# Kernel tuning notes

Hardware: AMD Instinct MI355X
Metric: run time of the kernel (lower is better)

The kernel has to match this reference:

```python
import jax, jax.numpy as jnp
import numpy as np

N_NODES = 100000


def _graph_conv(x, W, b, src, dst, norm):
    # DGL GraphConv(norm='left'): scale source features by 1/out_degree,
    # aggregate (sum over incoming edges). in_feats > out_feats so weight
    # multiply happens before aggregation (mathematically equivalent either way).
    h = x @ W  # [N, out]
    msg = (h * norm[:, None])[src]  # gather per-edge messages [E, out]
    agg = jax.ops.segment_sum(msg, dst, num_segments=N_NODES)
    return agg + b


def setup_inputs() -> dict:
    key = jax.random.key(0)
    ks = jax.random.split(key, 10)
    in_f, hid_f, out_f = 256, 128, 64
    n_edges = 1_600_000
    feat = jax.random.normal(ks[0], (N_NODES, in_f), dtype=jnp.float32)
    src = jax.random.randint(ks[1], (n_edges,), 0, N_NODES, dtype=jnp.int32)
    dst = jax.random.randint(ks[2], (n_edges,), 0, N_NODES, dtype=jnp.int32)
    noise = jax.random.normal(ks[3], (N_NODES, out_f), dtype=jnp.float32)
    s1 = 1.0 / np.sqrt(in_f)
    s2 = 1.0 / np.sqrt(hid_f)
    W_shared = jax.random.uniform(ks[4], (in_f, hid_f), minval=-s1, maxval=s1, dtype=jnp.float32)
    b_shared = jnp.zeros((hid_f,), jnp.float32)
    W_mu = jax.random.uniform(ks[5], (hid_f, out_f), minval=-s2, maxval=s2, dtype=jnp.float32)
    b_mu = jnp.zeros((out_f,), jnp.float32)
    W_ls = jax.random.uniform(ks[6], (hid_f, out_f), minval=-s2, maxval=s2, dtype=jnp.float32)
    b_ls = jnp.zeros((out_f,), jnp.float32)
    return {"feat": feat, "W_shared": W_shared, "b_shared": b_shared,
            "W_mu": W_mu, "b_mu": b_mu, "W_ls": W_ls, "b_ls": b_ls,
            "noise": noise, "src": src, "dst": dst}


def reference(feat, W_shared, b_shared, W_mu, b_mu, W_ls, b_ls, noise, src, dst):
    # left-norm: 1 / out_degree (clamped to >= 1, as DGL does)
    deg_out = jax.ops.segment_sum(jnp.ones_like(src, jnp.float32), src,
                                  num_segments=N_NODES)
    norm = 1.0 / jnp.maximum(deg_out, 1.0)
    # shared first GraphConv with ReLU activation
    h = jax.nn.relu(_graph_conv(feat, W_shared, b_shared, src, dst, norm))
    # two heads (no activation)
    mu = _graph_conv(h, W_mu, b_mu, src, dst, norm)
    log_sigma = _graph_conv(h, W_ls, b_ls, src, dst, norm)
    # reparameterized sample
    return mu + noise * jnp.exp(log_sigma)
```

## Files before the change

kernel.cpp:

```cpp
#include <hip/hip_runtime.h>
#include <hip/hip_bf16.h>
#include <math.h>

typedef __attribute__((ext_vector_type(8))) short short8;
typedef __attribute__((ext_vector_type(4))) float f32x4;

__device__ __forceinline__ unsigned short f2bf(float f) {
    unsigned int u = __float_as_uint(f);
    u += 0x7FFF + ((u >> 16) & 1);
    return (unsigned short)(u >> 16);
}
__device__ __forceinline__ float b2f(unsigned short s) {
    return __uint_as_float(((unsigned int)s) << 16);
}
__device__ __forceinline__ unsigned int f2bf2(float a, float b) {
    __hip_bfloat162 h = __float22bfloat162_rn(make_float2(a, b));
    return *(unsigned int*)&h;
}
__device__ __forceinline__ void gl_lds16(const void* g, void* l) {
    __builtin_amdgcn_global_load_lds(
        (const __attribute__((address_space(1))) void*)g,
        (__attribute__((address_space(3))) void*)l, 16, 0, 0);
}

#define EB 8192
#define BSH 10
#define NBKT 128

__global__ __launch_bounds__(256)
void k1_hist(const int* __restrict__ src, const int* __restrict__ dst,
             int* __restrict__ bhist, int E) {
    __shared__ int hist[256];
    int t = threadIdx.x;
    hist[t] = 0;
    __syncthreads();
    int base = blockIdx.x * EB;
    int end = min(base + EB, E);
    for (int e = base + 4 * t; e < end; e += 1024) {
        if (e + 3 < end) {
            int4 d4 = *(const int4*)&dst[e];
            int4 s4 = *(const int4*)&src[e];
            atomicAdd(&hist[d4.x >> BSH], 1);
            atomicAdd(&hist[d4.y >> BSH], 1);
            atomicAdd(&hist[d4.z >> BSH], 1);
            atomicAdd(&hist[d4.w >> BSH], 1);
            atomicAdd(&hist[128 + (s4.x >> BSH)], 1);
            atomicAdd(&hist[128 + (s4.y >> BSH)], 1);
            atomicAdd(&hist[128 + (s4.z >> BSH)], 1);
            atomicAdd(&hist[128 + (s4.w >> BSH)], 1);
        } else {
            for (int q = e; q < end; ++q) {
                atomicAdd(&hist[dst[q] >> BSH], 1);
                atomicAdd(&hist[128 + (src[q] >> BSH)], 1);
            }
        }
    }
    __syncthreads();
    bhist[(size_t)blockIdx.x * 256 + t] = hist[t];
}

__global__ __launch_bounds__(256)
void kc1_totals(const int* __restrict__ bhist, int* __restrict__ totals, int PB) {
    int t = threadIdx.x;
    int slice = (PB + 7) / 8;
    int b0 = blockIdx.x * slice;
    int b1 = min(b0 + slice, PB);
    int s = 0;
    for (int blk = b0; blk < b1; ++blk) s += bhist[(size_t)blk * 256 + t];
    if (s) atomicAdd(&totals[t], s);
}

__global__ __launch_bounds__(256)
void kc2_scan2(const int* __restrict__ totals, int* __restrict__ bbase_d,
               int* __restrict__ bbase_s) {
    __shared__ int s[256];
    int t = threadIdx.x;
    int v = totals[t];
    s[t] = v;
    __syncthreads();
    for (int off = 1; off < 128; off <<= 1) {
        int u = ((t & 127) >= off) ? s[t - off] : 0;
        __syncthreads();
        s[t] += u;
        __syncthreads();
    }
    int excl = s[t] - v;
    if (t < 128) bbase_d[t] = excl;
    else bbase_s[t - 128] = excl;
}

__global__ __launch_bounds__(256)
void kc3_boff(const int* __restrict__ bhist, const int* __restrict__ bbase_d,
              const int* __restrict__ bbase_s, int* __restrict__ boffT, int PB) {
    __shared__ int sums[256];
    int b = blockIdx.x;
    int t = threadIdx.x;
    int v = (t < PB) ? bhist[(size_t)t * 256 + b] : 0;
    sums[t] = v;
    __syncthreads();
    for (int off = 1; off < 256; off <<= 1) {
        int u = (t >= off) ? sums[t - off] : 0;
        __syncthreads();
        sums[t] += u;
        __syncthreads();
    }
    int base = (b < 128) ? bbase_d[b] : bbase_s[b - 128];
    if (t < PB) boffT[(size_t)b * PB + t] = base + sums[t] - v;
}

__global__ __launch_bounds__(256)
void k2_scatter(const int* __restrict__ src, const int* __restrict__ dst,
                const int* __restrict__ boffT, int2* __restrict__ parr,
                int* __restrict__ sarr, int E, int PB) {
    __shared__ int cnt[256];
    int t = threadIdx.x;
    int blk = blockIdx.x;
    cnt[t] = boffT[(size_t)t * PB + blk];
    __syncthreads();
    int base = blk * EB;
    int end = min(base + EB, E);
    for (int e = base + 4 * t; e < end; e += 1024) {
        if (e + 3 < end) {
            int4 s4 = *(const int4*)&src[e];
            int4 d4 = *(const int4*)&dst[e];
            int p0 = atomicAdd(&cnt[d4.x >> BSH], 1); parr[p0] = make_int2(s4.x, d4.x);
            int p1 = atomicAdd(&cnt[d4.y >> BSH], 1); parr[p1] = make_int2(s4.y, d4.y);
            int p2 = atomicAdd(&cnt[d4.z >> BSH], 1); parr[p2] = make_int2(s4.z, d4.z);
            int p3 = atomicAdd(&cnt[d4.w >> BSH], 1); parr[p3] = make_int2(s4.w, d4.w);
            int q0 = atomicAdd(&cnt[128 + (s4.x >> BSH)], 1); sarr[q0] = s4.x;
            int q1 = atomicAdd(&cnt[128 + (s4.y >> BSH)], 1); sarr[q1] = s4.y;
            int q2 = atomicAdd(&cnt[128 + (s4.z >> BSH)], 1); sarr[q2] = s4.z;
            int q3 = atomicAdd(&cnt[128 + (s4.w >> BSH)], 1); sarr[q3] = s4.w;
        } else {
            for (int q = e; q < end; ++q) {
                int sv = src[q], dv = dst[q];
                int pd = atomicAdd(&cnt[dv >> BSH], 1);
                parr[pd] = make_int2(sv, dv);
                int ps = atomicAdd(&cnt[128 + (sv >> BSH)], 1);
                sarr[ps] = sv;
            }
        }
    }
}

__global__ __launch_bounds__(1024)
void k3_dst(const int2* __restrict__ parr, const int* __restrict__ totals,
            const int* __restrict__ bbase_d, int* __restrict__ row_off,
            int* __restrict__ col, int N, int E) {
    __shared__ int hist[1024], sc[1024];
    int b = blockIdx.x, t = threadIdx.x;
    if (b == 0 && t == 0) row_off[N] = E;
    int ne = totals[b];
    int ebase = bbase_d[b];
    hist[t] = 0;
    __syncthreads();
    for (int i = t; i < ne; i += 1024)
        atomicAdd(&hist[parr[ebase + i].y & 1023], 1);
    __syncthreads();
    int h = hist[t];
    sc[t] = h;
    __syncthreads();
    for (int off = 1; off < 1024; off <<= 1) {
        int u = (t >= off) ? sc[t - off] : 0;
        __syncthreads();
        sc[t] += u;
        __syncthreads();
    }
    int excl = sc[t] - h;
    int node = b * 1024 + t;
    if (node < N) row_off[node] = ebase + excl;
    hist[t] = ebase + excl;
    __syncthreads();
    for (int i = t; i < ne; i += 1024) {
        int2 pr = parr[ebase + i];
        int slot = atomicAdd(&hist[pr.y & 1023], 1);
        col[slot] = pr.x;
    }
}

__global__ __launch_bounds__(1024)
void k3_src(const int* __restrict__ sarr, const int* __restrict__ totals_s,
            const int* __restrict__ bbase_s, float* __restrict__ norm, int N) {
    __shared__ int hist[1024];
    int b = blockIdx.x, t = threadIdx.x;
    int ne = totals_s[b];
    int sb = bbase_s[b];
    hist[t] = 0;
    __syncthreads();
    for (int i = t; i < ne; i += 1024)
        atomicAdd(&hist[sarr[sb + i] & 1023], 1);
    __syncthreads();
    int node = b * 1024 + t;
    if (node < N) {
        int d = hist[t];
        norm[node] = 1.0f / (float)(d > 1 ? d : 1);
    }
}

__global__ __launch_bounds__(256)
void k_wprep(const float* __restrict__ Wsh, const float* __restrict__ Wmu,
             const float* __restrict__ Wls, unsigned short* __restrict__ W1T,
             unsigned short* __restrict__ W2T) {
    int b = blockIdx.x, t = threadIdx.x;
    if (b < 128) {
        W1T[(size_t)b * 256 + t] = f2bf(Wsh[(size_t)t * 128 + b]);
    } else {
        int n = b - 128;
        if (t < 128) {
            float v = (n < 64) ? Wmu[(size_t)t * 64 + n]
                               : Wls[(size_t)t * 64 + (n - 64)];
            W2T[(size_t)n * 128 + t] = f2bf(v);
        }
    }
}

__global__ __launch_bounds__(256)
void k_gemm1(const float* __restrict__ A, int M,
             const unsigned short* __restrict__ W1T,
             const float* __restrict__ norm, unsigned short* __restrict__ outb) {
    __shared__ char ldsA[64 * 1040];
    const int w = threadIdx.x >> 6;
    const int lane = threadIdx.x & 63;
    const int quad = lane >> 4;
    const int l16 = lane & 15;
    const int cl = w * 16 + l16;
    const int r0 = blockIdx.x * 64;

#pragma unroll
    for (int i = 0; i < 16; ++i) {
        int row = r0 + w * 16 + i;
        if (row >= M) row = M - 1;
        const char* g = (const char*)A + (size_t)row * 1024 + lane * 16;
        char* l = ldsA + (w * 16 + i) * 1040 + lane * 16;
        gl_lds16(g, l);
    }

    short8 bw[2][8];
#pragma unroll
    for (int hf = 0; hf < 2; ++hf) {
        const unsigned short* wp = W1T + (size_t)(hf * 64 + cl) * 256 + quad * 8;
#pragma unroll
        for (int ks = 0; ks < 8; ++ks)
            bw[hf][ks] = *(const short8*)(wp + ks * 32);
    }
    __syncthreads();

    f32x4 acc[4][2];
#pragma unroll
    for (int m = 0; m < 4; ++m) {
        acc[m][0] = (f32x4){0.f, 0.f, 0.f, 0.f};
        acc[m][1] = (f32x4){0.f, 0.f, 0.f, 0.f};
    }
#pragma unroll
    for (int ks = 0; ks < 8; ++ks) {
#pragma unroll
        for (int m = 0; m < 4; ++m) {
            const float* pr = (const float*)(ldsA + (m * 16 + l16) * 1040 +
                                             (ks * 32 + quad * 8) * 4);
            float4 x = *(const float4*)pr;
            float4 y = *(const float4*)(pr + 4);
            union { short8 v; unsigned int u[4]; } c;
            c.u[0] = f2bf2(x.x, x.y);
            c.u[1] = f2bf2(x.z, x.w);
            c.u[2] = f2bf2(y.x, y.y);
            c.u[3] = f2bf2(y.z, y.w);
            acc[m][0] = __builtin_amdgcn_mfma_f32_16x16x32_bf16(bw[0][ks], c.v, acc[m][0], 0, 0, 0);
            acc[m][1] = __builtin_amdgcn_mfma_f32_16x16x32_bf16(bw[1][ks], c.v, acc[m][1], 0, 0, 0);
        }
    }
    const int colbase = w * 16 + quad * 4;
#pragma unroll
    for (int m = 0; m < 4; ++m) {
        int row = r0 + m * 16 + l16;
        if (row < M) {
            float nm = norm[row];
            ushort4 o0, o1;
            o0.x = f2bf(acc[m][0][0] * nm); o0.y = f2bf(acc[m][0][1] * nm);
            o0.z = f2bf(acc[m][0][2] * nm); o0.w = f2bf(acc[m][0][3] * nm);
            o1.x = f2bf(acc[m][1][0] * nm); o1.y = f2bf(acc[m][1][1] * nm);
            o1.z = f2bf(acc[m][1][2] * nm); o1.w = f2bf(acc[m][1][3] * nm);
            *(ushort4*)&outb[(size_t)row * 128 + colbase] = o0;
            *(ushort4*)&outb[(size_t)row * 128 + 64 + colbase] = o1;
        }
    }
}

__global__ __launch_bounds__(256)
void k_gemm2(const unsigned short* __restrict__ A, int M,
             const unsigned short* __restrict__ W2T,
             const float* __restrict__ norm, unsigned short* __restrict__ outb) {
    __shared__ char ldsB[16 * 1040];
    const int w = threadIdx.x >> 6;
    const int lane = threadIdx.x & 63;
    const int quad = lane >> 4;
    const int l16 = lane & 15;
    const int cl = w * 16 + l16;
    const int r0 = blockIdx.x * 64;

#pragma unroll
    for (int i = 0; i < 4; ++i) {
        int c = w * 4 + i;
        int crow = r0 + c * 4;
        if (crow + 4 > M) crow = M - 4;
        const char* g = (const char*)A + (size_t)crow * 256 + lane * 16;
        char* l = ldsB + c * 1040 + lane * 16;
        gl_lds16(g, l);
    }

    short8 bw[2][4];
#pragma unroll
    for (int hf = 0; hf < 2; ++hf) {
        const unsigned short* wp = W2T + (size_t)(hf * 64 + cl) * 128 + quad * 8;
#pragma unroll
        for (int ks = 0; ks < 4; ++ks)
            bw[hf][ks] = *(const short8*)(wp + ks * 32);
    }
    __syncthreads();

    f32x4 acc[4][2];
#pragma unroll
    for (int m = 0; m < 4; ++m) {
        acc[m][0] = (f32x4){0.f, 0.f, 0.f, 0.f};
        acc[m][1] = (f32x4){0.f, 0.f, 0.f, 0.f};
    }
#pragma unroll
    for (int ks = 0; ks < 4; ++ks) {
#pragma unroll
        for (int m = 0; m < 4; ++m) {
            int row = m * 16 + l16;
            short8 af = *(const short8*)(ldsB + (row >> 2) * 1040 + (row & 3) * 256 +
                                         (ks * 32 + quad * 8) * 2);
            acc[m][0] = __builtin_amdgcn_mfma_f32_16x16x32_bf16(bw[0][ks], af, acc[m][0], 0, 0, 0);
            acc[m][1] = __builtin_amdgcn_mfma_f32_16x16x32_bf16(bw[1][ks], af, acc[m][1], 0, 0, 0);
        }
    }
    const int colbase = w * 16 + quad * 4;
#pragma unroll
    for (int m = 0; m < 4; ++m) {
        int row = r0 + m * 16 + l16;
        if (row < M) {
            float nm = norm[row];
            ushort4 o0, o1;
            o0.x = f2bf(acc[m][0][0] * nm); o0.y = f2bf(acc[m][0][1] * nm);
            o0.z = f2bf(acc[m][0][2] * nm); o0.w = f2bf(acc[m][0][3] * nm);
            o1.x = f2bf(acc[m][1][0] * nm); o1.y = f2bf(acc[m][1][1] * nm);
            o1.z = f2bf(acc[m][1][2] * nm); o1.w = f2bf(acc[m][1][3] * nm);
            *(ushort4*)&outb[(size_t)row * 128 + colbase] = o0;
            *(ushort4*)&outb[(size_t)row * 128 + 64 + colbase] = o1;
        }
    }
}

__global__ __launch_bounds__(256)
void k_spmm_relu(const int* __restrict__ row_off, const int* __restrict__ col,
                 const unsigned short* __restrict__ hxb, const float* __restrict__ bias,
                 unsigned short* __restrict__ hb, int N) {
    int g = (blockIdx.x * blockDim.x + threadIdx.x) >> 5;
    int l = threadIdx.x & 31;
    if (g >= N) return;
    int e0 = row_off[g], e1 = row_off[g + 1];
    const ushort4* base = (const ushort4*)hxb;
    float4 acc = make_float4(0.f, 0.f, 0.f, 0.f);
    int e = e0;
    for (; e + 7 < e1; e += 8) {
        ushort4 v0 = base[(size_t)col[e] * 32 + l];
        ushort4 v1 = base[(size_t)col[e + 1] * 32 + l];
        ushort4 v2 = base[(size_t)col[e + 2] * 32 + l];
        ushort4 v3 = base[(size_t)col[e + 3] * 32 + l];
        ushort4 v4 = base[(size_t)col[e + 4] * 32 + l];
        ushort4 v5 = base[(size_t)col[e + 5] * 32 + l];
        ushort4 v6 = base[(size_t)col[e + 6] * 32 + l];
        ushort4 v7 = base[(size_t)col[e + 7] * 32 + l];
        acc.x += ((b2f(v0.x) + b2f(v1.x)) + (b2f(v2.x) + b2f(v3.x))) +
                 ((b2f(v4.x) + b2f(v5.x)) + (b2f(v6.x) + b2f(v7.x)));
        acc.y += ((b2f(v0.y) + b2f(v1.y)) + (b2f(v2.y) + b2f(v3.y))) +
                 ((b2f(v4.y) + b2f(v5.y)) + (b2f(v6.y) + b2f(v7.y)));
        acc.z += ((b2f(v0.z) + b2f(v1.z)) + (b2f(v2.z) + b2f(v3.z))) +
                 ((b2f(v4.z) + b2f(v5.z)) + (b2f(v6.z) + b2f(v7.z)));
        acc.w += ((b2f(v0.w) + b2f(v1.w)) + (b2f(v2.w) + b2f(v3.w))) +
                 ((b2f(v4.w) + b2f(v5.w)) + (b2f(v6.w) + b2f(v7.w)));
    }
    for (; e + 1 < e1; e += 2) {
        ushort4 a = base[(size_t)col[e] * 32 + l];
        ushort4 b = base[(size_t)col[e + 1] * 32 + l];
        acc.x += b2f(a.x) + b2f(b.x);
        acc.y += b2f(a.y) + b2f(b.y);
        acc.z += b2f(a.z) + b2f(b.z);
        acc.w += b2f(a.w) + b2f(b.w);
    }
    if (e < e1) {
        ushort4 a = base[(size_t)col[e] * 32 + l];
        acc.x += b2f(a.x); acc.y += b2f(a.y); acc.z += b2f(a.z); acc.w += b2f(a.w);
    }
    float4 bi = ((const float4*)bias)[l];
    ushort4 r;
    r.x = f2bf(fmaxf(acc.x + bi.x, 0.f));
    r.y = f2bf(fmaxf(acc.y + bi.y, 0.f));
    r.z = f2bf(fmaxf(acc.z + bi.z, 0.f));
    r.w = f2bf(fmaxf(acc.w + bi.w, 0.f));
    ((ushort4*)hb)[(size_t)g * 32 + l] = r;
}

__global__ __launch_bounds__(256)
void k_spmm_out(const int* __restrict__ row_off, const int* __restrict__ col,
                const unsigned short* __restrict__ hcb, const float* __restrict__ bmu,
                const float* __restrict__ bls, const float* __restrict__ noise,
                float* __restrict__ out, int N) {
    int g = (blockIdx.x * blockDim.x + threadIdx.x) >> 5;
    int l = threadIdx.x & 31;
    if (g >= N) return;
    int e0 = row_off[g], e1 = row_off[g + 1];
    const ushort4* base = (const ushort4*)hcb;
    float4 acc = make_float4(0.f, 0.f, 0.f, 0.f);
    int e = e0;
    for (; e + 7 < e1; e += 8) {
        ushort4 v0 = base[(size_t)col[e] * 32 + l];
        ushort4 v1 = base[(size_t)col[e + 1] * 32 + l];
        ushort4 v2 = base[(size_t)col[e + 2] * 32 + l];
        ushort4 v3 = base[(size_t)col[e + 3] * 32 + l];
        ushort4 v4 = base[(size_t)col[e + 4] * 32 + l];
        ushort4 v5 = base[(size_t)col[e + 5] * 32 + l];
        ushort4 v6 = base[(size_t)col[e + 6] * 32 + l];
        ushort4 v7 = base[(size_t)col[e + 7] * 32 + l];
        acc.x += ((b2f(v0.x) + b2f(v1.x)) + (b2f(v2.x) + b2f(v3.x))) +
                 ((b2f(v4.x) + b2f(v5.x)) + (b2f(v6.x) + b2f(v7.x)));
        acc.y += ((b2f(v0.y) + b2f(v1.y)) + (b2f(v2.y) + b2f(v3.y))) +
                 ((b2f(v4.y) + b2f(v5.y)) + (b2f(v6.y) + b2f(v7.y)));
        acc.z += ((b2f(v0.z) + b2f(v1.z)) + (b2f(v2.z) + b2f(v3.z))) +
                 ((b2f(v4.z) + b2f(v5.z)) + (b2f(v6.z) + b2f(v7.z)));
        acc.w += ((b2f(v0.w) + b2f(v1.w)) + (b2f(v2.w) + b2f(v3.w))) +
                 ((b2f(v4.w) + b2f(v5.w)) + (b2f(v6.w) + b2f(v7.w)));
    }
    for (; e + 1 < e1; e += 2) {
        ushort4 a = base[(size_t)col[e] * 32 + l];
        ushort4 b = base[(size_t)col[e + 1] * 32 + l];
        acc.x += b2f(a.x) + b2f(b.x);
        acc.y += b2f(a.y) + b2f(b.y);
        acc.z += b2f(a.z) + b2f(b.z);
        acc.w += b2f(a.w) + b2f(b.w);
    }
    if (e < e1) {
        ushort4 a = base[(size_t)col[e] * 32 + l];
        acc.x += b2f(a.x); acc.y += b2f(a.y); acc.z += b2f(a.z); acc.w += b2f(a.w);
    }
    int lane64 = threadIdx.x & 63;
    int p = (lane64 + 16) & 63;
    float lx = __shfl(acc.x, p, 64);
    float ly = __shfl(acc.y, p, 64);
    float lz = __shfl(acc.z, p, 64);
    float lw = __shfl(acc.w, p, 64);
    if (l < 16) {
        float4 bm = ((const float4*)bmu)[l];
        float4 bl = ((const float4*)bls)[l];
        float4 nz = ((const float4*)noise)[(size_t)g * 16 + l];
        float4 o;
        o.x = (acc.x + bm.x) + nz.x * expf(lx + bl.x);
        o.y = (acc.y + bm.y) + nz.y * expf(ly + bl.y);
        o.z = (acc.z + bm.z) + nz.z * expf(lz + bl.z);
        o.w = (acc.w + bm.w) + nz.w * expf(lw + bl.w);
        ((float4*)out)[(size_t)g * 16 + l] = o;
    }
}

static inline char* align64(char* p) {
    return (char*)(((uintptr_t)p + 63) & ~(uintptr_t)63);
}

extern "C" void kernel_launch(void* const* d_in, const int* in_sizes, int n_in,
                              void* d_out, int out_size, void* d_ws, size_t ws_size,
                              hipStream_t stream) {
    const float* feat  = (const float*)d_in[0];
    const float* Wsh   = (const float*)d_in[1];
    const float* bsh   = (const float*)d_in[2];
    const float* Wmu   = (const float*)d_in[3];
    const float* bmu   = (const float*)d_in[4];
    const float* Wls   = (const float*)d_in[5];
    const float* bls   = (const float*)d_in[6];
    const float* noise = (const float*)d_in[7];
    const int*   src   = (const int*)d_in[8];
    const int*   dst   = (const int*)d_in[9];
    float* out = (float*)d_out;

    const int N = in_sizes[0] / 256;
    const int E = in_sizes[8];
    const int PB = (E + EB - 1) / EB;

    char* p = (char*)d_ws;
    float* norm   = (float*)p;                  p += (size_t)N * 4;         p = align64(p);
    int* row_off  = (int*)p;                    p += (size_t)(N + 4) * 4;   p = align64(p);
    int* totals   = (int*)p;                    p += 256 * 4;
    int* bbase_d  = (int*)p;                    p += 128 * 4;
    int* bbase_s  = (int*)p;                    p += 128 * 4;               p = align64(p);
    unsigned short* W1T = (unsigned short*)p;   p += (size_t)128 * 256 * 2;
    unsigned short* W2T = (unsigned short*)p;   p += (size_t)128 * 128 * 2;
    p = align64(p);
    int* bhist    = (int*)p;                    p += (size_t)PB * 256 * 4;  p = align64(p);
    int* boffT    = (int*)p;                    p += (size_t)256 * PB * 4;  p = align64(p);
    int2* parr    = (int2*)p;                   p += (size_t)E * 8;
    int* sarr     = (int*)p;                    p += (size_t)E * 4;
    int* col      = (int*)p;                    p += (size_t)E * 4;         p = align64(p);
    unsigned short* hxb = (unsigned short*)p;
    unsigned short* hb  = (unsigned short*)d_out;

    hipMemsetAsync(totals, 0, 256 * sizeof(int), stream);
    k_wprep<<<256, 256, 0, stream>>>(Wsh, Wmu, Wls, W1T, W2T);
    k1_hist<<<PB, 256, 0, stream>>>(src, dst, bhist, E);
    kc1_totals<<<8, 256, 0, stream>>>(bhist, totals, PB);
    kc2_scan2<<<1, 256, 0, stream>>>(totals, bbase_d, bbase_s);
    kc3_boff<<<256, 256, 0, stream>>>(bhist, bbase_d, bbase_s, boffT, PB);
    k2_scatter<<<PB, 256, 0, stream>>>(src, dst, boffT, parr, sarr, E, PB);
    k3_dst<<<NBKT, 1024, 0, stream>>>(parr, totals, bbase_d, row_off, col, N, E);
    k3_src<<<NBKT, 1024, 0, stream>>>(sarr, totals + 128, bbase_s, norm, N);

    int gtiles = (N + 63) / 64;
    k_gemm1<<<gtiles, 256, 0, stream>>>(feat, N, W1T, norm, hxb);
    k_spmm_relu<<<(N * 32 + 255) / 256, 256, 0, stream>>>(row_off, col, hxb, bsh, hb, N);
    k_gemm2<<<gtiles, 256, 0, stream>>>(hb, N, W2T, norm, hxb);
    k_spmm_out<<<(N * 32 + 255) / 256, 256, 0, stream>>>(row_off, col, hxb, bmu, bls, noise, out, N);
}
```

Baseline: 450.0 us.

## Use 256 finer CSR buckets, pack edge pairs into 32 bits, merge scan kernels

Bucket width for the CSR build drops from 1024 to 512 nodes, giving 256 dst/src buckets so the per-bucket kernels launch more, smaller blocks. Edge pairs are packed into one int (17-bit src plus 9-bit local dst) and the src-degree array stores only 16-bit local ids, cutting scatter write traffic and later read traffic. The totals reduction and bucket scan are merged into one single-block kernel, removing a memset and a launch. The packing assumes node ids fit in 17 bits and the merged kernel runs on only one block, which may serialize the reduction over bhist.

```diff
diff --git a/kernel.cpp b/kernel.cpp
--- a/kernel.cpp
+++ b/kernel.cpp
@@ -24,15 +24,15 @@
 }
 
 #define EB 8192
-#define BSH 10
-#define NBKT 128
+#define BSH 9
+#define NBKT 256
 
 __global__ __launch_bounds__(256)
 void k1_hist(const int* __restrict__ src, const int* __restrict__ dst,
              int* __restrict__ bhist, int E) {
-    __shared__ int hist[256];
+    __shared__ int hist[512];
     int t = threadIdx.x;
-    hist[t] = 0;
+    hist[t] = 0; hist[t + 256] = 0;
     __syncthreads();
     int base = blockIdx.x * EB;
     int end = min(base + EB, E);
@@ -44,49 +44,54 @@
             atomicAdd(&hist[d4.y >> BSH], 1);
             atomicAdd(&hist[d4.z >> BSH], 1);
             atomicAdd(&hist[d4.w >> BSH], 1);
-            atomicAdd(&hist[128 + (s4.x >> BSH)], 1);
-            atomicAdd(&hist[128 + (s4.y >> BSH)], 1);
-            atomicAdd(&hist[128 + (s4.z >> BSH)], 1);
-            atomicAdd(&hist[128 + (s4.w >> BSH)], 1);
+            atomicAdd(&hist[256 + (s4.x >> BSH)], 1);
+            atomicAdd(&hist[256 + (s4.y >> BSH)], 1);
+            atomicAdd(&hist[256 + (s4.z >> BSH)], 1);
+            atomicAdd(&hist[256 + (s4.w >> BSH)], 1);
         } else {
             for (int q = e; q < end; ++q) {
                 atomicAdd(&hist[dst[q] >> BSH], 1);
-                atomicAdd(&hist[128 + (src[q] >> BSH)], 1);
+                atomicAdd(&hist[256 + (src[q] >> BSH)], 1);
             }
         }
     }
     __syncthreads();
-    bhist[(size_t)blockIdx.x * 256 + t] = hist[t];
-}
-
-__global__ __launch_bounds__(256)
-void kc1_totals(const int* __restrict__ bhist, int* __restrict__ totals, int PB) {
+    int* o = bhist + (size_t)blockIdx.x * 512;
+    o[t] = hist[t];
+    o[t + 256] = hist[t + 256];
+}
+
+__global__ __launch_bounds__(1024)
+void kc12(const int* __restrict__ bhist, int* __restrict__ totals,
+          int* __restrict__ bbase_d, int* __restrict__ bbase_s, int PB) {
+    __shared__ int part[1024];
+    __shared__ int s[512];
     int t = threadIdx.x;
-    int slice = (PB + 7) / 8;
-    int b0 = blockIdx.x * slice;
-    int b1 = min(b0 + slice, PB);
-    int s = 0;
-    for (int blk = b0; blk < b1; ++blk) s += bhist[(size_t)blk * 256 + t];
-    if (s) atomicAdd(&totals[t], s);
-}
-
-__global__ __launch_bounds__(256)
-void kc2_scan2(const int* __restrict__ totals, int* __restrict__ bbase_d,
-               int* __restrict__ bbase_s) {
-    __shared__ int s[256];
-    int t = threadIdx.x;
-    int v = totals[t];
-    s[t] = v;
-    __syncthreads();
-    for (int off = 1; off < 128; off <<= 1) {
-        int u = ((t & 127) >= off) ? s[t - off] : 0;
+    int bin = t & 511, half = t >> 9;
+    int sum = 0;
+    for (int blk = half; blk < PB; blk += 2)
+        sum += bhist[(size_t)blk * 512 + bin];
+    part[t] = sum;
+    __syncthreads();
+    int v = 0;
+    if (t < 512) {
+        v = part[t] + part[t + 512];
+        totals[t] = v;
+        s[t] = v;
+    }
+    __syncthreads();
+    for (int off = 1; off < 256; off <<= 1) {
+        int u = 0;
+        if (t < 512 && (t & 255) >= off) u = s[t - off];
         __syncthreads();
-        s[t] += u;
+        if (t < 512) s[t] += u;
         __syncthreads();
     }
-    int excl = s[t] - v;
-    if (t < 128) bbase_d[t] = excl;
-    else bbase_s[t - 128] = excl;
+    if (t < 512) {
+        int excl = s[t] - v;
+        if (t < 256) bbase_d[t] = excl;
+        else bbase_s[t - 256] = excl;
+    }
 }
 
 __global__ __launch_bounds__(256)
@@ -95,7 +100,7 @@
     __shared__ int sums[256];
     int b = blockIdx.x;
     int t = threadIdx.x;
-    int v = (t < PB) ? bhist[(size_t)t * 256 + b] : 0;
+    int v = (t < PB) ? bhist[(size_t)t * 512 + b] : 0;
     sums[t] = v;
     __syncthreads();
     for (int off = 1; off < 256; off <<= 1) {
@@ -104,18 +109,19 @@
         sums[t] += u;
         __syncthreads();
     }
-    int base = (b < 128) ? bbase_d[b] : bbase_s[b - 128];
+    int base = (b < 256) ? bbase_d[b] : bbase_s[b - 256];
     if (t < PB) boffT[(size_t)b * PB + t] = base + sums[t] - v;
 }
 
 __global__ __launch_bounds__(256)
 void k2_scatter(const int* __restrict__ src, const int* __restrict__ dst,
-                const int* __restrict__ boffT, int2* __restrict__ parr,
-                int* __restrict__ sarr, int E, int PB) {
-    __shared__ int cnt[256];
+                const int* __restrict__ boffT, int* __restrict__ parr,
+                unsigned short* __restrict__ sarr, int E, int PB) {
+    __shared__ int cnt[512];
     int t = threadIdx.x;
     int blk = blockIdx.x;
     cnt[t] = boffT[(size_t)t * PB + blk];
+    cnt[t + 256] = boffT[(size_t)(t + 256) * PB + blk];
     __syncthreads();
     int base = blk * EB;
     int end = min(base + EB, E);
@@ -123,74 +129,74 @@
         if (e + 3 < end) {
             int4 s4 = *(const int4*)&src[e];
             int4 d4 = *(const int4*)&dst[e];
-            int p0 = atomicAdd(&cnt[d4.x >> BSH], 1); parr[p0] = make_int2(s4.x, d4.x);
-            int p1 = atomicAdd(&cnt[d4.y >> BSH], 1); parr[p1] = make_int2(s4.y, d4.y);
-            int p2 = atomicAdd(&cnt[d4.z >> BSH], 1); parr[p2] = make_int2(s4.z, d4.z);
-            int p3 = atomicAdd(&cnt[d4.w >> BSH], 1); parr[p3] = make_int2(s4.w, d4.w);
-            int q0 = atomicAdd(&cnt[128 + (s4.x >> BSH)], 1); sarr[q0] = s4.x;
-            int q1 = atomicAdd(&cnt[128 + (s4.y >> BSH)], 1); sarr[q1] = s4.y;
-            int q2 = atomicAdd(&cnt[128 + (s4.z >> BSH)], 1); sarr[q2] = s4.z;
-            int q3 = atomicAdd(&cnt[128 + (s4.w >> BSH)], 1); sarr[q3] = s4.w;
+            int p0 = atomicAdd(&cnt[d4.x >> BSH], 1); parr[p0] = s4.x | ((d4.x & 511) << 17);
+            int p1 = atomicAdd(&cnt[d4.y >> BSH], 1); parr[p1] = s4.y | ((d4.y & 511) << 17);
+            int p2 = atomicAdd(&cnt[d4.z >> BSH], 1); parr[p2] = s4.z | ((d4.z & 511) << 17);
+            int p3 = atomicAdd(&cnt[d4.w >> BSH], 1); parr[p3] = s4.w | ((d4.w & 511) << 17);
+            int q0 = atomicAdd(&cnt[256 + (s4.x >> BSH)], 1); sarr[q0] = (unsigned short)(s4.x & 511);
+            int q1 = atomicAdd(&cnt[256 + (s4.y >> BSH)], 1); sarr[q1] = (unsigned short)(s4.y & 511);
+            int q2 = atomicAdd(&cnt[256 + (s4.z >> BSH)], 1); sarr[q2] = (unsigned short)(s4.z & 511);
+            int q3 = atomicAdd(&cnt[256 + (s4.w >> BSH)], 1); sarr[q3] = (unsigned short)(s4.w & 511);
         } else {
             for (int q = e; q < end; ++q) {
                 int sv = src[q], dv = dst[q];
                 int pd = atomicAdd(&cnt[dv >> BSH], 1);
-                parr[pd] = make_int2(sv, dv);
-                int ps = atomicAdd(&cnt[128 + (sv >> BSH)], 1);
-                sarr[ps] = sv;
+                parr[pd] = sv | ((dv & 511) << 17);
+                int ps = atomicAdd(&cnt[256 + (sv >> BSH)], 1);
+                sarr[ps] = (unsigned short)(sv & 511);
             }
         }
     }
 }
 
-__global__ __launch_bounds__(1024)
-void k3_dst(const int2* __restrict__ parr, const int* __restrict__ totals,
+__global__ __launch_bounds__(512)
+void k3_dst(const int* __restrict__ parr, const int* __restrict__ totals,
             const int* __restrict__ bbase_d, int* __restrict__ row_off,
             int* __restrict__ col, int N, int E) {
-    __shared__ int hist[1024], sc[1024];
+    __shared__ int hist[512], sc[512];
     int b = blockIdx.x, t = threadIdx.x;
     if (b == 0 && t == 0) row_off[N] = E;
     int ne = totals[b];
     int ebase = bbase_d[b];
     hist[t] = 0;
     __syncthreads();
-    for (int i = t; i < ne; i += 1024)
-        atomicAdd(&hist[parr[ebase + i].y & 1023], 1);
+    for (int i = t; i < ne; i += 512)
+        atomicAdd(&hist[(parr[ebase + i] >> 17) & 511], 1);
     __syncthreads();
     int h = hist[t];
     sc[t] = h;
     __syncthreads();
-    for (int off = 1; off < 1024; off <<= 1) {
+    for (int off = 1; off < 512; off <<= 1) {
         int u = (t >= off) ? sc[t - off] : 0;
         __syncthreads();
         sc[t] += u;
         __syncthreads();
     }
     int excl = sc[t] - h;
-    int node = b * 1024 + t;
+    int node = b * 512 + t;
     if (node < N) row_off[node] = ebase + excl;
     hist[t] = ebase + excl;
     __syncthreads();
-    for (int i = t; i < ne; i += 1024) {
-        int2 pr = parr[ebase + i];
-        int slot = atomicAdd(&hist[pr.y & 1023], 1);
-        col[slot] = pr.x;
-    }
-}
-
-__global__ __launch_bounds__(1024)
-void k3_src(const int* __restrict__ sarr, const int* __restrict__ totals_s,
+    for (int i = t; i < ne; i += 512) {
+        int v = parr[ebase + i];
+        int slot = atomicAdd(&hist[(v >> 17) & 511], 1);
+        col[slot] = v & 0x1FFFF;
+    }
+}
+
+__global__ __launch_bounds__(512)
+void k3_src(const unsigned short* __restrict__ sarr, const int* __restrict__ totals_s,
             const int* __restrict__ bbase_s, float* __restrict__ norm, int N) {
-    __shared__ int hist[1024];
+    __shared__ int hist[512];
     int b = blockIdx.x, t = threadIdx.x;
     int ne = totals_s[b];
     int sb = bbase_s[b];
     hist[t] = 0;
     __syncthreads();
-    for (int i = t; i < ne; i += 1024)
-        atomicAdd(&hist[sarr[sb + i] & 1023], 1);
-    __syncthreads();
-    int node = b * 1024 + t;
+    for (int i = t; i < ne; i += 512)
+        atomicAdd(&hist[sarr[sb + i]], 1);
+    __syncthreads();
+    int node = b * 512 + t;
     if (node < N) {
         int d = hist[t];
         norm[node] = 1.0f / (float)(d > 1 ? d : 1);
@@ -488,29 +494,27 @@
     char* p = (char*)d_ws;
     float* norm   = (float*)p;                  p += (size_t)N * 4;         p = align64(p);
     int* row_off  = (int*)p;                    p += (size_t)(N + 4) * 4;   p = align64(p);
-    int* totals   = (int*)p;                    p += 256 * 4;
-    int* bbase_d  = (int*)p;                    p += 128 * 4;
-    int* bbase_s  = (int*)p;                    p += 128 * 4;               p = align64(p);
+    int* totals   = (int*)p;                    p += 512 * 4;
+    int* bbase_d  = (int*)p;                    p += 256 * 4;
+    int* bbase_s  = (int*)p;                    p += 256 * 4;               p = align64(p);
     unsigned short* W1T = (unsigned short*)p;   p += (size_t)128 * 256 * 2;
     unsigned short* W2T = (unsigned short*)p;   p += (size_t)128 * 128 * 2;
     p = align64(p);
-    int* bhist    = (int*)p;                    p += (size_t)PB * 256 * 4;  p = align64(p);
-    int* boffT    = (int*)p;                    p += (size_t)256 * PB * 4;  p = align64(p);
-    int2* parr    = (int2*)p;                   p += (size_t)E * 8;
-    int* sarr     = (int*)p;                    p += (size_t)E * 4;
+    int* bhist    = (int*)p;                    p += (size_t)PB * 512 * 4;  p = align64(p);
+    int* boffT    = (int*)p;                    p += (size_t)512 * PB * 4;  p = align64(p);
+    int* parr     = (int*)p;                    p += (size_t)E * 4;
+    unsigned short* sarr = (unsigned short*)p;  p += (size_t)E * 2;         p = align64(p);
     int* col      = (int*)p;                    p += (size_t)E * 4;         p = align64(p);
     unsigned short* hxb = (unsigned short*)p;
     unsigned short* hb  = (unsigned short*)d_out;
 
-    hipMemsetAsync(totals, 0, 256 * sizeof(int), stream);
     k_wprep<<<256, 256, 0, stream>>>(Wsh, Wmu, Wls, W1T, W2T);
     k1_hist<<<PB, 256, 0, stream>>>(src, dst, bhist, E);
-    kc1_totals<<<8, 256, 0, stream>>>(bhist, totals, PB);
-    kc2_scan2<<<1, 256, 0, stream>>>(totals, bbase_d, bbase_s);
-    kc3_boff<<<256, 256, 0, stream>>>(bhist, bbase_d, bbase_s, boffT, PB);
+    kc12<<<1, 1024, 0, stream>>>(bhist, totals, bbase_d, bbase_s, PB);
+    kc3_boff<<<512, 256, 0, stream>>>(bhist, bbase_d, bbase_s, boffT, PB);
     k2_scatter<<<PB, 256, 0, stream>>>(src, dst, boffT, parr, sarr, E, PB);
-    k3_dst<<<NBKT, 1024, 0, stream>>>(parr, totals, bbase_d, row_off, col, N, E);
-    k3_src<<<NBKT, 1024, 0, stream>>>(sarr, totals + 128, bbase_s, norm, N);
+    k3_dst<<<NBKT, 512, 0, stream>>>(parr, totals, bbase_d, row_off, col, N, E);
+    k3_src<<<NBKT, 512, 0, stream>>>(sarr, totals + 256, bbase_s, norm, N);
 
     int gtiles = (N + 63) / 64;
     k_gemm1<<<gtiles, 256, 0, stream>>>(feat, N, W1T, norm, hxb);
```

Measured after the change: 450.8 us. No clear change (+0.2%).
